# Optimization experiments

Hardware: AMD Instinct MI355X
Metric: run time of the kernel (lower is better)

The kernel has to match this reference:

```python
import jax, jax.numpy as jnp
import numpy as np

B, C, D, TOPK = 4096, 8192, 128, 10


def calc_distmat2(x, y):
    d = (x * x).sum(-1)[:, None] + (y * y).sum(-1)[None, :] - 2.0 * (x @ y.T)
    return jnp.clip(d, 1e-12, 1e12)


def setup_inputs() -> dict:
    key = jax.random.key(0)
    k1, k2, k3 = jax.random.split(key, 3)
    x = jax.random.normal(k1, (B, D), dtype=jnp.float32)
    labels = jax.random.randint(k2, (B,), 0, C)
    # kaiming_normal_(mode='fan_out') on (C, D): fan_out = C, gain = sqrt(2)
    centers = jax.random.normal(k3, (C, D), dtype=jnp.float32) * np.float32(np.sqrt(2.0 / C))
    return {"x": x, "labels": labels, "centers": centers, "topk": TOPK}


def reference(x, labels, centers, topk):
    num_classes = centers.shape[0]
    distmat = calc_distmat2(x, centers)                      # (B, C)
    lab = labels[:, None]                                    # (B, 1)
    dist_pull = jnp.take_along_axis(distmat, lab, axis=1)[:, 0]  # (B,)
    loss_pull = dist_pull.mean()

    # mode 'exp': per-row masked topk over negatives + log-softmax over [pos, neg_topk]
    logits = -distmat                                        # (B, C)
    pos = jnp.take_along_axis(logits, lab, axis=1)           # (B, 1)
    is_pos = lab == jnp.arange(num_classes)[None, :]         # (B, C)
    neg_logits = jnp.where(is_pos, -jnp.inf, logits)
    neg_topk, _ = jax.lax.top_k(neg_logits, topk)            # (B, topk)
    cat = jnp.concatenate([pos, neg_topk], axis=1)           # (B, 1+topk)
    # -log_softmax at index 0 (the positive) per row, averaged ('ccent')
    loss = (-jax.nn.log_softmax(cat, axis=1)[:, 0]).mean()

    # center-to-center repulsion over strictly-lower-triangular pairs
    cent2cent = calc_distmat2(centers, centers)              # (C, C)
    tri = jnp.tril(jnp.ones((num_classes, num_classes), dtype=bool), -1)
    n_pairs = num_classes * (num_classes - 1) // 2
    loss_dis = -jnp.sum(jnp.where(tri, cent2cent, 0.0)) / jnp.float32(n_pairs)

    return (loss, loss_dis, cent2cent, loss_pull)
```

## Files before the change

### kernel.cpp

```cpp
#include <hip/hip_runtime.h>
#include <hip/hip_bf16.h>
#include <math.h>

#define NB 4096
#define NC 8192
#define ND 128
#define NSPLIT 16
#define CPS (NC / NSPLIT)
#define NTILES (CPS / 16)
#define XBLKS (64 * NSPLIT)

#define WS_XN 16
#define WS_CN (WS_XN + NB)
#define WS_POS (WS_CN + NC)
#define WS_PART (WS_POS + NB)
#define WS_XB (WS_PART + NB * NSPLIT * 10)
#define WS_CB (WS_XB + NB * ND / 2)

typedef __attribute__((ext_vector_type(8))) short short8v;
typedef __attribute__((ext_vector_type(4))) float f32x4;

__global__ __launch_bounds__(256) void prep_kernel(
    const float* __restrict__ x, const float* __restrict__ c, float* __restrict__ ws) {
  if (blockIdx.x == 0 && threadIdx.x < 16) ws[threadIdx.x] = 0.0f;
  int wid = threadIdx.x >> 6, lane = threadIdx.x & 63;
  int row = blockIdx.x * 4 + wid;
  const float* src;
  float* ndst;
  ushort* bdst;
  if (row < NB) {
    src = x + (size_t)row * ND;
    ndst = ws + WS_XN + row;
    bdst = (ushort*)(ws + WS_XB) + (size_t)row * ND;
  } else {
    int r = row - NB;
    src = c + (size_t)r * ND;
    ndst = ws + WS_CN + r;
    bdst = (ushort*)(ws + WS_CB) + (size_t)r * ND;
  }
  float2 v = *(const float2*)(src + lane * 2);
  __hip_bfloat16 h0 = __float2bfloat16(v.x);
  __hip_bfloat16 h1 = __float2bfloat16(v.y);
  ushort2 u;
  u.x = *(ushort*)&h0;
  u.y = *(ushort*)&h1;
  *(ushort2*)(bdst + lane * 2) = u;
  float s = fmaf(v.x, v.x, v.y * v.y);
#pragma unroll
  for (int off = 32; off; off >>= 1) s += __shfl_down(s, off, 64);
  if (lane == 0) *ndst = s;
}

#define INS10(arr, val)                          \
  {                                              \
    float _v = (val);                            \
    _Pragma("unroll") for (int _k = 0; _k < 10; ++_k) { \
      float _mx = fmaxf(arr[_k], _v);            \
      _v = fminf(arr[_k], _v);                   \
      arr[_k] = _mx;                             \
    }                                            \
  }

__global__ __launch_bounds__(256) void mega_kernel(
    const int* __restrict__ labels, float* __restrict__ ws, float* __restrict__ outmat) {
  int t = threadIdx.x;
  int w = t >> 6, l = t & 63, lo = l & 15, hi = l >> 4;
  int bid = blockIdx.x;

  if (bid < XBLKS) {
    int split = bid >> 6;
    int row = (bid & 63) * 64 + w * 16 + lo;
    int cbase = split * CPS;
    const ushort* xb = (const ushort*)(ws + WS_XB);
    const ushort* cb = (const ushort*)(ws + WS_CB);

    const ushort* xrp = xb + (size_t)row * ND + hi * 8;
    short8v xf0 = *(const short8v*)(xrp + 0);
    short8v xf1 = *(const short8v*)(xrp + 32);
    short8v xf2 = *(const short8v*)(xrp + 64);
    short8v xf3 = *(const short8v*)(xrp + 96);

    float xn = ws[WS_XN + row];
    int lab = labels[row];

    float top[10];
#pragma unroll
    for (int k = 0; k < 10; ++k) top[k] = -3.0e38f;
    float posv = -3.0e38f;

    for (int tl = 0; tl < NTILES; ++tl) {
      int c0 = cbase + tl * 16;
      const ushort* cp = cb + (size_t)(c0 + lo) * ND + hi * 8;
      short8v a0 = *(const short8v*)(cp + 0);
      short8v a1 = *(const short8v*)(cp + 32);
      short8v a2 = *(const short8v*)(cp + 64);
      short8v a3 = *(const short8v*)(cp + 96);
      f32x4 acc = {0.f, 0.f, 0.f, 0.f};
      acc = __builtin_amdgcn_mfma_f32_16x16x32_bf16(a0, xf0, acc, 0, 0, 0);
      acc = __builtin_amdgcn_mfma_f32_16x16x32_bf16(a1, xf1, acc, 0, 0, 0);
      acc = __builtin_amdgcn_mfma_f32_16x16x32_bf16(a2, xf2, acc, 0, 0, 0);
      acc = __builtin_amdgcn_mfma_f32_16x16x32_bf16(a3, xf3, acc, 0, 0, 0);

      f32x4 cn4 = *(const f32x4*)(ws + WS_CN + c0 + hi * 4);
#pragma unroll
      for (int r = 0; r < 4; ++r) {
        int cidx = c0 + hi * 4 + r;
        float dist = xn + cn4[r] - 2.0f * acc[r];
        dist = fminf(fmaxf(dist, 1e-12f), 1e12f);
        float s = -dist;
        bool isl = (cidx == lab);
        posv = isl ? s : posv;
        float se = isl ? -3.0e38f : s;
        INS10(top, se)
      }
    }

    float oth[10];
#pragma unroll
    for (int m = 16; m <= 32; m <<= 1) {
#pragma unroll
      for (int k = 0; k < 10; ++k) oth[k] = __shfl_xor(top[k], m, 64);
#pragma unroll
      for (int k = 0; k < 10; ++k) INS10(top, oth[k])
    }

    if (posv > -1.0e37f) ws[WS_POS + row] = posv;
    if (hi == 0) {
      float* dst = ws + WS_PART + ((size_t)row * NSPLIT + split) * 10;
#pragma unroll
      for (int k = 0; k < 10; ++k) dst[k] = top[k];
    }
  } else {
    int bid2 = bid - XBLKS;
    int bi = bid2 >> 6, bj = bid2 & 63;
    int wm = w >> 1, wn = w & 1;
    int rowb = bi * 128 + wm * 64;
    int colb = bj * 128 + wn * 64;
    const ushort* cb = (const ushort*)(ws + WS_CB);

    f32x4 acc[4][4];
#pragma unroll
    for (int m = 0; m < 4; ++m)
#pragma unroll
      for (int n = 0; n < 4; ++n) acc[m][n] = (f32x4){0.f, 0.f, 0.f, 0.f};

#pragma unroll
    for (int ks = 0; ks < 4; ++ks) {
      short8v af[4], bf[4];
#pragma unroll
      for (int m = 0; m < 4; ++m)
        af[m] = *(const short8v*)(cb + (size_t)(rowb + m * 16 + lo) * ND + ks * 32 + hi * 8);
#pragma unroll
      for (int n = 0; n < 4; ++n)
        bf[n] = *(const short8v*)(cb + (size_t)(colb + n * 16 + lo) * ND + ks * 32 + hi * 8);
#pragma unroll
      for (int m = 0; m < 4; ++m)
#pragma unroll
        for (int n = 0; n < 4; ++n)
          acc[m][n] = __builtin_amdgcn_mfma_f32_16x16x32_bf16(af[m], bf[n], acc[m][n], 0, 0, 0);
    }

    float cnj[4];
#pragma unroll
    for (int n = 0; n < 4; ++n) cnj[n] = ws[WS_CN + colb + n * 16 + lo];
    float tsum = 0.0f;
#pragma unroll
    for (int m = 0; m < 4; ++m) {
      f32x4 cni = *(const f32x4*)(ws + WS_CN + rowb + m * 16 + hi * 4);
#pragma unroll
      for (int n = 0; n < 4; ++n) {
#pragma unroll
        for (int rr = 0; rr < 4; ++rr) {
          int gr = rowb + m * 16 + hi * 4 + rr;
          int gc = colb + n * 16 + lo;
          float dd = cni[rr] + cnj[n] - 2.0f * acc[m][n][rr];
          dd = fminf(fmaxf(dd, 1e-12f), 1e12f);
          outmat[(size_t)gr * NC + gc] = dd;
          if (bi > bj) tsum += dd;
          else if (bi == bj) tsum += (gr > gc) ? dd : 0.0f;
        }
      }
    }

    __shared__ float red[4];
#pragma unroll
    for (int off = 32; off; off >>= 1) tsum += __shfl_down(tsum, off, 64);
    if (l == 0) red[w] = tsum;
    __syncthreads();
    if (t == 0) atomicAdd(ws + 1, red[0] + red[1] + red[2] + red[3]);
  }
}

__global__ __launch_bounds__(256) void merge_fin_kernel(float* __restrict__ ws,
                                                        float* __restrict__ out) {
  int row = blockIdx.x * 256 + threadIdx.x;
  const f32x4* part = (const f32x4*)(ws + WS_PART + (size_t)row * NSPLIT * 10);
  float top[10];
#pragma unroll
  for (int k = 0; k < 10; ++k) top[k] = -3.0e38f;
#pragma unroll
  for (int i = 0; i < NSPLIT * 10 / 4; ++i) {
    f32x4 v = part[i];
    INS10(top, v.x)
    INS10(top, v.y)
    INS10(top, v.z)
    INS10(top, v.w)
  }
  float pos = ws[WS_POS + row];
  float mx = fmaxf(pos, top[0]);
  float ssum = expf(pos - mx);
#pragma unroll
  for (int k = 0; k < 10; ++k) ssum += expf(top[k] - mx);
  float lrow = mx + logf(ssum) - pos;
  float prow = -pos;
#pragma unroll
  for (int off = 32; off; off >>= 1) {
    lrow += __shfl_down(lrow, off, 64);
    prow += __shfl_down(prow, off, 64);
  }
  if ((threadIdx.x & 63) == 0) {
    atomicAdd(ws + 0, lrow);
    atomicAdd(ws + 2, prow);
  }
  __syncthreads();
  if (threadIdx.x == 0) {
    __threadfence();
    unsigned tk = atomicAdd((unsigned int*)(ws + 3), 1u);
    if (tk == 15u) {
      float ls = atomicAdd(ws + 0, 0.0f);
      float ts = atomicAdd(ws + 1, 0.0f);
      float ps = atomicAdd(ws + 2, 0.0f);
      out[0] = ls / 4096.0f;
      out[1] = -ts / 33550336.0f;
      out[2 + (size_t)NC * NC] = ps / 4096.0f;
    }
  }
}

extern "C" void kernel_launch(void* const* d_in, const int* in_sizes, int n_in,
                              void* d_out, int out_size, void* d_ws, size_t ws_size,
                              hipStream_t stream) {
  const float* x = (const float*)d_in[0];
  const int* labels = (const int*)d_in[1];
  const float* centers = (const float*)d_in[2];
  float* out = (float*)d_out;
  float* ws = (float*)d_ws;

  hipLaunchKernelGGL(prep_kernel, dim3((NB + NC) / 4), dim3(256), 0, stream, x, centers, ws);
  hipLaunchKernelGGL(mega_kernel, dim3(XBLKS + 64 * 64), dim3(256), 0, stream, labels, ws, out + 2);
  hipLaunchKernelGGL(merge_fin_kernel, dim3(NB / 256), dim3(256), 0, stream, ws, out);
}
```

Before: 182.9 us.

## Split fused kernel and stage center-distance tiles through LDS for coalesced stores

Splits the combined launch into a separate top-k loss kernel and a center-to-center distance kernel. The distance kernel uses 128x64 tiles, computes values into a padded shared-memory tile, then writes full contiguous row segments with 16-byte vector stores instead of scattered 64-byte column fragments. The aim is to cut the cost of writing the large output matrix, which limits the run. The trade-offs are extra LDS use, a barrier before the stores, and losing the overlap between the two workloads that the single launch allowed.

Result: slower. 215.7 us (+18.0%).

```diff
diff --git a/kernel.cpp b/kernel.cpp
--- a/kernel.cpp
+++ b/kernel.cpp
@@ -8,7 +8,6 @@
 #define NSPLIT 16
 #define CPS (NC / NSPLIT)
 #define NTILES (CPS / 16)
-#define XBLKS (64 * NSPLIT)
 
 #define WS_XN 16
 #define WS_CN (WS_XN + NB)
@@ -61,133 +60,145 @@
     }                                            \
   }
 
-__global__ __launch_bounds__(256) void mega_kernel(
-    const int* __restrict__ labels, float* __restrict__ ws, float* __restrict__ outmat) {
+__global__ __launch_bounds__(256) void xloss_kernel(
+    const int* __restrict__ labels, float* __restrict__ ws) {
   int t = threadIdx.x;
   int w = t >> 6, l = t & 63, lo = l & 15, hi = l >> 4;
-  int bid = blockIdx.x;
-
-  if (bid < XBLKS) {
-    int split = bid >> 6;
-    int row = (bid & 63) * 64 + w * 16 + lo;
-    int cbase = split * CPS;
-    const ushort* xb = (const ushort*)(ws + WS_XB);
-    const ushort* cb = (const ushort*)(ws + WS_CB);
-
-    const ushort* xrp = xb + (size_t)row * ND + hi * 8;
-    short8v xf0 = *(const short8v*)(xrp + 0);
-    short8v xf1 = *(const short8v*)(xrp + 32);
-    short8v xf2 = *(const short8v*)(xrp + 64);
-    short8v xf3 = *(const short8v*)(xrp + 96);
-
-    float xn = ws[WS_XN + row];
-    int lab = labels[row];
-
-    float top[10];
-#pragma unroll
-    for (int k = 0; k < 10; ++k) top[k] = -3.0e38f;
-    float posv = -3.0e38f;
-
-    for (int tl = 0; tl < NTILES; ++tl) {
-      int c0 = cbase + tl * 16;
-      const ushort* cp = cb + (size_t)(c0 + lo) * ND + hi * 8;
-      short8v a0 = *(const short8v*)(cp + 0);
-      short8v a1 = *(const short8v*)(cp + 32);
-      short8v a2 = *(const short8v*)(cp + 64);
-      short8v a3 = *(const short8v*)(cp + 96);
-      f32x4 acc = {0.f, 0.f, 0.f, 0.f};
-      acc = __builtin_amdgcn_mfma_f32_16x16x32_bf16(a0, xf0, acc, 0, 0, 0);
-      acc = __builtin_amdgcn_mfma_f32_16x16x32_bf16(a1, xf1, acc, 0, 0, 0);
-      acc = __builtin_amdgcn_mfma_f32_16x16x32_bf16(a2, xf2, acc, 0, 0, 0);
-      acc = __builtin_amdgcn_mfma_f32_16x16x32_bf16(a3, xf3, acc, 0, 0, 0);
-
-      f32x4 cn4 = *(const f32x4*)(ws + WS_CN + c0 + hi * 4);
-#pragma unroll
-      for (int r = 0; r < 4; ++r) {
-        int cidx = c0 + hi * 4 + r;
-        float dist = xn + cn4[r] - 2.0f * acc[r];
-        dist = fminf(fmaxf(dist, 1e-12f), 1e12f);
-        float s = -dist;
-        bool isl = (cidx == lab);
-        posv = isl ? s : posv;
-        float se = isl ? -3.0e38f : s;
-        INS10(top, se)
+  int row = blockIdx.x * 64 + w * 16 + lo;
+  int split = blockIdx.y;
+  int cbase = split * CPS;
+
+  const ushort* xb = (const ushort*)(ws + WS_XB);
+  const ushort* cb = (const ushort*)(ws + WS_CB);
+
+  const ushort* xrp = xb + (size_t)row * ND + hi * 8;
+  short8v xf0 = *(const short8v*)(xrp + 0);
+  short8v xf1 = *(const short8v*)(xrp + 32);
+  short8v xf2 = *(const short8v*)(xrp + 64);
+  short8v xf3 = *(const short8v*)(xrp + 96);
+
+  float xn = ws[WS_XN + row];
+  int lab = labels[row];
+
+  float top[10];
+#pragma unroll
+  for (int k = 0; k < 10; ++k) top[k] = -3.0e38f;
+  float posv = -3.0e38f;
+
+  for (int tl = 0; tl < NTILES; ++tl) {
+    int c0 = cbase + tl * 16;
+    const ushort* cp = cb + (size_t)(c0 + lo) * ND + hi * 8;
+    short8v a0 = *(const short8v*)(cp + 0);
+    short8v a1 = *(const short8v*)(cp + 32);
+    short8v a2 = *(const short8v*)(cp + 64);
+    short8v a3 = *(const short8v*)(cp + 96);
+    f32x4 acc = {0.f, 0.f, 0.f, 0.f};
+    acc = __builtin_amdgcn_mfma_f32_16x16x32_bf16(a0, xf0, acc, 0, 0, 0);
+    acc = __builtin_amdgcn_mfma_f32_16x16x32_bf16(a1, xf1, acc, 0, 0, 0);
+    acc = __builtin_amdgcn_mfma_f32_16x16x32_bf16(a2, xf2, acc, 0, 0, 0);
+    acc = __builtin_amdgcn_mfma_f32_16x16x32_bf16(a3, xf3, acc, 0, 0, 0);
+
+    f32x4 cn4 = *(const f32x4*)(ws + WS_CN + c0 + hi * 4);
+#pragma unroll
+    for (int r = 0; r < 4; ++r) {
+      int cidx = c0 + hi * 4 + r;
+      float dist = xn + cn4[r] - 2.0f * acc[r];
+      dist = fminf(fmaxf(dist, 1e-12f), 1e12f);
+      float s = -dist;
+      bool isl = (cidx == lab);
+      posv = isl ? s : posv;
+      float se = isl ? -3.0e38f : s;
+      INS10(top, se)
+    }
+  }
+
+  float oth[10];
+#pragma unroll
+  for (int m = 16; m <= 32; m <<= 1) {
+#pragma unroll
+    for (int k = 0; k < 10; ++k) oth[k] = __shfl_xor(top[k], m, 64);
+#pragma unroll
+    for (int k = 0; k < 10; ++k) INS10(top, oth[k])
+  }
+
+  if (posv > -1.0e37f) ws[WS_POS + row] = posv;
+  if (hi == 0) {
+    float* dst = ws + WS_PART + ((size_t)row * NSPLIT + split) * 10;
+#pragma unroll
+    for (int k = 0; k < 10; ++k) dst[k] = top[k];
+  }
+}
+
+__global__ __launch_bounds__(256) void c2c_kernel(
+    float* __restrict__ ws, float* __restrict__ outmat) {
+  __shared__ float tile[128][65];
+  __shared__ float red[4];
+  int bi = blockIdx.x;
+  int bj = blockIdx.y;
+  int t = threadIdx.x;
+  int w = t >> 6, l = t & 63, lo = l & 15, hi = l >> 4;
+  int wm = w >> 1, wn = w & 1;
+  int rowb = bi * 128 + wm * 64;
+  int colb = bj * 64 + wn * 32;
+  const ushort* cb = (const ushort*)(ws + WS_CB);
+
+  f32x4 acc[4][2];
+#pragma unroll
+  for (int m = 0; m < 4; ++m)
+#pragma unroll
+    for (int n = 0; n < 2; ++n) acc[m][n] = (f32x4){0.f, 0.f, 0.f, 0.f};
+
+#pragma unroll
+  for (int ks = 0; ks < 4; ++ks) {
+    short8v af[4], bf[2];
+#pragma unroll
+    for (int m = 0; m < 4; ++m)
+      af[m] = *(const short8v*)(cb + (size_t)(rowb + m * 16 + lo) * ND + ks * 32 + hi * 8);
+#pragma unroll
+    for (int n = 0; n < 2; ++n)
+      bf[n] = *(const short8v*)(cb + (size_t)(colb + n * 16 + lo) * ND + ks * 32 + hi * 8);
+#pragma unroll
+    for (int m = 0; m < 4; ++m)
+#pragma unroll
+      for (int n = 0; n < 2; ++n)
+        acc[m][n] = __builtin_amdgcn_mfma_f32_16x16x32_bf16(af[m], bf[n], acc[m][n], 0, 0, 0);
+  }
+
+  float cnj[2];
+#pragma unroll
+  for (int n = 0; n < 2; ++n) cnj[n] = ws[WS_CN + colb + n * 16 + lo];
+  float tsum = 0.0f;
+#pragma unroll
+  for (int m = 0; m < 4; ++m) {
+    f32x4 cni = *(const f32x4*)(ws + WS_CN + rowb + m * 16 + hi * 4);
+#pragma unroll
+    for (int n = 0; n < 2; ++n) {
+#pragma unroll
+      for (int rr = 0; rr < 4; ++rr) {
+        int lr = wm * 64 + m * 16 + hi * 4 + rr;
+        int lc = wn * 32 + n * 16 + lo;
+        int gr = bi * 128 + lr;
+        int gc = bj * 64 + lc;
+        float dd = cni[rr] + cnj[n] - 2.0f * acc[m][n][rr];
+        dd = fminf(fmaxf(dd, 1e-12f), 1e12f);
+        tsum += (gr > gc) ? dd : 0.0f;
+        tile[lr][lc] = dd;
       }
     }
-
-    float oth[10];
-#pragma unroll
-    for (int m = 16; m <= 32; m <<= 1) {
-#pragma unroll
-      for (int k = 0; k < 10; ++k) oth[k] = __shfl_xor(top[k], m, 64);
-#pragma unroll
-      for (int k = 0; k < 10; ++k) INS10(top, oth[k])
-    }
-
-    if (posv > -1.0e37f) ws[WS_POS + row] = posv;
-    if (hi == 0) {
-      float* dst = ws + WS_PART + ((size_t)row * NSPLIT + split) * 10;
-#pragma unroll
-      for (int k = 0; k < 10; ++k) dst[k] = top[k];
-    }
-  } else {
-    int bid2 = bid - XBLKS;
-    int bi = bid2 >> 6, bj = bid2 & 63;
-    int wm = w >> 1, wn = w & 1;
-    int rowb = bi * 128 + wm * 64;
-    int colb = bj * 128 + wn * 64;
-    const ushort* cb = (const ushort*)(ws + WS_CB);
-
-    f32x4 acc[4][4];
-#pragma unroll
-    for (int m = 0; m < 4; ++m)
-#pragma unroll
-      for (int n = 0; n < 4; ++n) acc[m][n] = (f32x4){0.f, 0.f, 0.f, 0.f};
-
-#pragma unroll
-    for (int ks = 0; ks < 4; ++ks) {
-      short8v af[4], bf[4];
-#pragma unroll
-      for (int m = 0; m < 4; ++m)
-        af[m] = *(const short8v*)(cb + (size_t)(rowb + m * 16 + lo) * ND + ks * 32 + hi * 8);
-#pragma unroll
-      for (int n = 0; n < 4; ++n)
-        bf[n] = *(const short8v*)(cb + (size_t)(colb + n * 16 + lo) * ND + ks * 32 + hi * 8);
-#pragma unroll
-      for (int m = 0; m < 4; ++m)
-#pragma unroll
-        for (int n = 0; n < 4; ++n)
-          acc[m][n] = __builtin_amdgcn_mfma_f32_16x16x32_bf16(af[m], bf[n], acc[m][n], 0, 0, 0);
-    }
-
-    float cnj[4];
-#pragma unroll
-    for (int n = 0; n < 4; ++n) cnj[n] = ws[WS_CN + colb + n * 16 + lo];
-    float tsum = 0.0f;
-#pragma unroll
-    for (int m = 0; m < 4; ++m) {
-      f32x4 cni = *(const f32x4*)(ws + WS_CN + rowb + m * 16 + hi * 4);
-#pragma unroll
-      for (int n = 0; n < 4; ++n) {
-#pragma unroll
-        for (int rr = 0; rr < 4; ++rr) {
-          int gr = rowb + m * 16 + hi * 4 + rr;
-          int gc = colb + n * 16 + lo;
-          float dd = cni[rr] + cnj[n] - 2.0f * acc[m][n][rr];
-          dd = fminf(fmaxf(dd, 1e-12f), 1e12f);
-          outmat[(size_t)gr * NC + gc] = dd;
-          if (bi > bj) tsum += dd;
-          else if (bi == bj) tsum += (gr > gc) ? dd : 0.0f;
-        }
-      }
-    }
-
-    __shared__ float red[4];
-#pragma unroll
-    for (int off = 32; off; off >>= 1) tsum += __shfl_down(tsum, off, 64);
-    if (l == 0) red[w] = tsum;
-    __syncthreads();
-    if (t == 0) atomicAdd(ws + 1, red[0] + red[1] + red[2] + red[3]);
+  }
+
+#pragma unroll
+  for (int off = 32; off; off >>= 1) tsum += __shfl_down(tsum, off, 64);
+  if (l == 0) red[w] = tsum;
+  __syncthreads();
+  if (t == 0) atomicAdd(ws + 1, red[0] + red[1] + red[2] + red[3]);
+
+  int tr0 = t >> 4, c4 = (t & 15) << 2;
+  float* ob = outmat + (size_t)(bi * 128) * NC + bj * 64 + c4;
+#pragma unroll
+  for (int p = 0; p < 8; ++p) {
+    int tr = p * 16 + tr0;
+    *(f32x4*)(ob + (size_t)tr * NC) = *(const f32x4*)&tile[tr][c4];
   }
 }
 
@@ -247,6 +258,7 @@
   float* ws = (float*)d_ws;
 
   hipLaunchKernelGGL(prep_kernel, dim3((NB + NC) / 4), dim3(256), 0, stream, x, centers, ws);
-  hipLaunchKernelGGL(mega_kernel, dim3(XBLKS + 64 * 64), dim3(256), 0, stream, labels, ws, out + 2);
+  hipLaunchKernelGGL(xloss_kernel, dim3(64, NSPLIT), dim3(256), 0, stream, labels, ws);
+  hipLaunchKernelGGL(c2c_kernel, dim3(64, 128), dim3(256), 0, stream, ws, out + 2);
   hipLaunchKernelGGL(merge_fin_kernel, dim3(NB / 256), dim3(256), 0, stream, ws, out);
 }
```
